# Performance work log

Hardware: AMD Instinct MI355X
Metric: run time of the kernel (lower is better)

Reference implementation:

```python
import jax, jax.numpy as jnp
import numpy as np

LEAKY_SLOPE = 0.01  # torch F.leaky_relu default
LN_EPS = 1e-5       # torch nn.LayerNorm default


def _layer_norm(x, g, b):
    mu = jnp.mean(x, axis=-1, keepdims=True)
    var = jnp.var(x, axis=-1, keepdims=True)
    return (x - mu) * jax.lax.rsqrt(var + LN_EPS) * g + b


def _gcn(x, adj, W, b):
    # GraphConvolution (Kipf-style): adj @ (x @ W) + b
    return adj @ (x @ W) + b


def setup_inputs() -> dict:
    key = jax.random.key(0)
    ks = jax.random.split(key, 8)
    N, fan_in, fan_mid, fan_out = 12288, 128, 128, 20
    h0, h1, h2 = fan_mid, fan_mid // 2, fan_mid // 4  # 128, 64, 32
    inp = {
        "x": jax.random.normal(ks[0], (N, fan_in), dtype=jnp.float32),
        "adj0": jax.random.uniform(ks[1], (N, N), dtype=jnp.float32),
        "adj1": jax.random.uniform(ks[2], (N, N), dtype=jnp.float32),
        "adj2": jax.random.uniform(ks[3], (N, N), dtype=jnp.float32),
        "W0": jax.random.normal(ks[4], (fan_in, h0), dtype=jnp.float32) / np.sqrt(fan_in),
        "b0": jnp.zeros((h0,), dtype=jnp.float32),
        "W1": jax.random.normal(ks[5], (h0, h1), dtype=jnp.float32) / np.sqrt(h0),
        "b1": jnp.zeros((h1,), dtype=jnp.float32),
        "W2": jax.random.normal(ks[6], (h1, h2), dtype=jnp.float32) / np.sqrt(h1),
        "b2": jnp.zeros((h2,), dtype=jnp.float32),
        "g0": jnp.ones((h0,), dtype=jnp.float32),
        "be0": jnp.zeros((h0,), dtype=jnp.float32),
        "g1": jnp.ones((h1,), dtype=jnp.float32),
        "be1": jnp.zeros((h1,), dtype=jnp.float32),
        "g2": jnp.ones((h2,), dtype=jnp.float32),
        "be2": jnp.zeros((h2,), dtype=jnp.float32),
        "Wl": jax.random.normal(ks[7], (h2, fan_out), dtype=jnp.float32) / np.sqrt(h2),
        "bl": jnp.zeros((fan_out,), dtype=jnp.float32),
    }
    return inp


def reference(x, adj0, adj1, adj2, W0, b0, W1, b1, W2, b2,
              g0, be0, g1, be1, g2, be2, Wl, bl):
    # first GCN + LayerNorm (no activation, matching the original forward)
    h = _layer_norm(_gcn(x, adj0, W0, b0), g0, be0)
    # two loop iterations: GCN -> LN -> LeakyReLU -> Dropout(eval=identity)
    h = jax.nn.leaky_relu(_layer_norm(_gcn(h, adj1, W1, b1), g1, be1), LEAKY_SLOPE)
    h = jax.nn.leaky_relu(_layer_norm(_gcn(h, adj2, W2, b2), g2, be2), LEAKY_SLOPE)
    logits = h @ Wl + bl
    return jax.nn.log_softmax(logits, axis=1)
```

## Files before the change

kernel.cpp:

```cpp
#include <hip/hip_runtime.h>
#include <cstdint>
#include <cstddef>

typedef __attribute__((ext_vector_type(8))) short short8;
typedef __attribute__((ext_vector_type(4))) float f32x4;

#define DEV __device__ __forceinline__

DEV unsigned short f2bf(float f) {
  unsigned int u = __float_as_uint(f);
  u += 0x7fffu + ((u >> 16) & 1u);
  return (unsigned short)(u >> 16);
}

DEV unsigned int pk2(float a, float b) {
  return (unsigned int)f2bf(a) | ((unsigned int)f2bf(b) << 16);
}

DEV void glds16(const void* g, void* l) {
  __builtin_amdgcn_global_load_lds(
      (const __attribute__((address_space(1))) void*)g,
      (__attribute__((address_space(3))) void*)l, 16, 0, 0);
}

constexpr int NROW = 12288;

__global__ __launch_bounds__(256) void xw_kernel(
    const float* __restrict__ x, const float* __restrict__ W0,
    unsigned short* __restrict__ t0T) {
  __shared__ float sW[128 * 128];
  __shared__ float sx[16][128];
  const int t = threadIdx.x;
  for (int i = t; i < 128 * 128; i += 256) sW[i] = W0[i];
  const int r0 = blockIdx.x * 16;
  for (int i = t; i < 16 * 128; i += 256)
    sx[i >> 7][i & 127] = x[(size_t)(r0 + (i >> 7)) * 128 + (i & 127)];
  __syncthreads();
  const int c = t & 127;
  const int rg = t >> 7;
  float acc[8] = {0, 0, 0, 0, 0, 0, 0, 0};
  for (int k = 0; k < 128; ++k) {
    float w = sW[k * 128 + c];
#pragma unroll
    for (int j = 0; j < 8; ++j) acc[j] += sx[rg * 8 + j][k] * w;
  }
  uint4 o;
  o.x = pk2(acc[0], acc[1]);
  o.y = pk2(acc[2], acc[3]);
  o.z = pk2(acc[4], acc[5]);
  o.w = pk2(acc[6], acc[7]);
  *(uint4*)(t0T + (size_t)c * NROW + r0 + rg * 8) = o;
}

template <int H>
__global__ __launch_bounds__(256, 3) void gcn_gemm(
    const float* __restrict__ A, const unsigned short* __restrict__ BT,
    float* __restrict__ part) {
  constexpr int KSPLIT = 4;
  constexpr int BM = 64, BK = 64;
  constexpr int WN = (H >= 64) ? 2 : 1;
  constexpr int WM = 4 / WN;
  constexpr int MR = BM / (WM * 16);
  constexpr int NR = H / (WN * 16);
  constexpr int NB = H / 32;
  constexpr int KSTEPS = (NROW / KSPLIT) / BK;
  constexpr int NSUP = KSTEPS / 3;
  constexpr int BBYTES = H * 128;
  static_assert(KSTEPS % 3 == 0, "");

  __shared__ alignas(16) char lds[16384 + 2 * BBYTES];
  char* ldsB = lds + 16384;

  const int t = threadIdx.x;
  const int xcd = blockIdx.x & 7;
  const int idx = blockIdx.x >> 3;
  const int split = xcd >> 1;
  const int bm = ((xcd & 1) ? 96 : 0) + idx;
  const int k0 = split * (NROW / KSPLIT);

  const int r = t >> 2, q = t & 3;
  const float* aptr = A + (size_t)(bm * BM + r) * NROW + k0;
  const int sw = (r & 7) << 4;

  const int nB0 = t >> 3;
  const int wB = (t & 7) ^ (nB0 & 7);
  const unsigned short* bptr = BT + (size_t)nB0 * NROW + k0 + wB * 8;
  const int wid = t >> 6;
  char* ldsBw = ldsB + wid * 1024;

  const int lane = t & 63;
  const int l15 = lane & 15;
  const int loct = lane >> 4;
  const int wm = wid / WN;
  const int wn = wid % WN;
  int aoff[MR][2], boff[NR][2];
#pragma unroll
  for (int m = 0; m < MR; ++m)
#pragma unroll
    for (int kk = 0; kk < 2; ++kk) {
      int row = wm * (MR * 16) + m * 16 + l15;
      aoff[m][kk] = (row * 128 + kk * 64 + loct * 16) ^ ((row & 7) << 4);
    }
#pragma unroll
  for (int n = 0; n < NR; ++n)
#pragma unroll
    for (int kk = 0; kk < 2; ++kk) {
      int nn = wn * (NR * 16) + n * 16 + l15;
      boff[n][kk] = (nn * 128 + kk * 64 + loct * 16) ^ ((nn & 7) << 4);
    }

  f32x4 acc[MR][NR];
#pragma unroll
  for (int m = 0; m < MR; ++m)
#pragma unroll
    for (int n = 0; n < NR; ++n) acc[m][n] = {0.f, 0.f, 0.f, 0.f};

  f32x4 av[12];

  auto issueSuper = [&](int S) {
#pragma unroll
    for (int j = 0; j < 3; ++j)
#pragma unroll
      for (int i = 0; i < 4; ++i)
        av[j * 4 + i] =
            *(const f32x4*)(aptr + S * 192 + j * 64 + i * 16 + q * 4);
  };
  auto glB = [&](int s, int buf) {
#pragma unroll
    for (int j = 0; j < NB; ++j)
      glds16(bptr + (size_t)j * 32 * NROW + s * BK,
             ldsBw + buf * BBYTES + j * 4096);
  };
  auto cvtWrite = [&](int j, int buf) {
    char* wb = lds + buf * 8192;
#pragma unroll
    for (int i = 0; i < 4; ++i) {
      uint2 w;
      w.x = pk2(av[j * 4 + i].x, av[j * 4 + i].y);
      w.y = pk2(av[j * 4 + i].z, av[j * 4 + i].w);
      *(uint2*)(wb + ((r * 128 + i * 32 + q * 8) ^ sw)) = w;
    }
  };
  auto compute = [&](int buf) {
    const char* lA = lds + buf * 8192;
    const char* lB = ldsB + buf * BBYTES;
#pragma unroll
    for (int kk = 0; kk < 2; ++kk) {
      short8 af[MR], bfv[NR];
#pragma unroll
      for (int m = 0; m < MR; ++m) af[m] = *(const short8*)(lA + aoff[m][kk]);
#pragma unroll
      for (int n = 0; n < NR; ++n) bfv[n] = *(const short8*)(lB + boff[n][kk]);
#pragma unroll
      for (int m = 0; m < MR; ++m)
#pragma unroll
        for (int n = 0; n < NR; ++n)
          acc[m][n] = __builtin_amdgcn_mfma_f32_16x16x32_bf16(
              af[m], bfv[n], acc[m][n], 0, 0, 0);
    }
  };

  glB(0, 0);
  __builtin_amdgcn_sched_barrier(0);
  issueSuper(0);
  cvtWrite(0, 0);
  asm volatile("s_waitcnt vmcnt(0) lgkmcnt(0)" ::: "memory");
  __builtin_amdgcn_s_barrier();
  __builtin_amdgcn_sched_barrier(0);

  for (int S = 0; S < NSUP; ++S) {
    const int b = S & 1;
    glB(3 * S + 1, b ^ 1);
    compute(b);
    cvtWrite(1, b ^ 1);
    asm volatile("s_waitcnt vmcnt(0) lgkmcnt(0)" ::: "memory");
    __builtin_amdgcn_s_barrier();
    __builtin_amdgcn_sched_barrier(0);
    glB(3 * S + 2, b);
    __builtin_amdgcn_sched_barrier(0);
    compute(b ^ 1);
    cvtWrite(2, b);
    if (S + 1 < NSUP) {
      issueSuper(S + 1);
      asm volatile("s_waitcnt vmcnt(12) lgkmcnt(0)" ::: "memory");
    } else {
      asm volatile("s_waitcnt vmcnt(0) lgkmcnt(0)" ::: "memory");
    }
    __builtin_amdgcn_s_barrier();
    __builtin_amdgcn_sched_barrier(0);
    if (S + 1 < NSUP) {
      glB(3 * S + 3, b ^ 1);
      compute(b);
      cvtWrite(0, b ^ 1);
      asm volatile("s_waitcnt vmcnt(0) lgkmcnt(0)" ::: "memory");
      __builtin_amdgcn_s_barrier();
      __builtin_amdgcn_sched_barrier(0);
    } else {
      compute(b);
    }
  }

  float* pout = part + ((size_t)split * NROW + (size_t)bm * BM) * H;
#pragma unroll
  for (int m = 0; m < MR; ++m) {
    const int row = wm * (MR * 16) + m * 16 + loct * 4;
#pragma unroll
    for (int n = 0; n < NR; ++n) {
      const int col = wn * (NR * 16) + n * 16 + l15;
#pragma unroll
      for (int rr = 0; rr < 4; ++rr)
        pout[(size_t)(row + rr) * H + col] = acc[m][n][rr];
    }
  }
}

template <int H, int H2, bool ACT>
__global__ __launch_bounds__(256) void reduce_ln(
    const float* __restrict__ part, const float* __restrict__ bias,
    const float* __restrict__ g, const float* __restrict__ be,
    const float* __restrict__ Wn, unsigned short* __restrict__ tT) {
  __shared__ float sW[H * H2];
  __shared__ float sh[4][H];
  const int t = threadIdx.x;
  for (int i = t; i < H * H2; i += 256) sW[i] = Wn[i];
  __syncthreads();

  const int wid = t >> 6, lane = t & 63;
  const int row = blockIdx.x * 4 + wid;
  constexpr int CPL = H / 64;
  float v[CPL];
#pragma unroll
  for (int c = 0; c < CPL; ++c) {
    const int col = lane + c * 64;
    float s = bias[col];
#pragma unroll
    for (int sp = 0; sp < 4; ++sp)
      s += part[((size_t)sp * NROW + row) * H + col];
    v[c] = s;
  }
  float sum = 0;
#pragma unroll
  for (int c = 0; c < CPL; ++c) sum += v[c];
#pragma unroll
  for (int o = 32; o > 0; o >>= 1) sum += __shfl_xor(sum, o);
  const float mu = sum / H;
  float vs = 0;
#pragma unroll
  for (int c = 0; c < CPL; ++c) { float d = v[c] - mu; vs += d * d; }
#pragma unroll
  for (int o = 32; o > 0; o >>= 1) vs += __shfl_xor(vs, o);
  const float rstd = rsqrtf(vs / H + 1e-5f);
#pragma unroll
  for (int c = 0; c < CPL; ++c) {
    const int col = lane + c * 64;
    float h = (v[c] - mu) * rstd * g[col] + be[col];
    if (ACT) h = (h > 0.f) ? h : 0.01f * h;
    sh[wid][col] = h;
  }
  __syncthreads();
  if (lane < H2) {
    float d = 0;
#pragma unroll 8
    for (int k = 0; k < H; ++k) d += sh[wid][k] * sW[k * H2 + lane];
    tT[(size_t)lane * NROW + row] = f2bf(d);
  }
}

__global__ __launch_bounds__(256) void reduce_final(
    const float* __restrict__ part, const float* __restrict__ bias,
    const float* __restrict__ g, const float* __restrict__ be,
    const float* __restrict__ Wl, const float* __restrict__ bl,
    float* __restrict__ out) {
  __shared__ float sW[32 * 20];
  __shared__ float sbl[20];
  __shared__ float sh[4][32];
  __shared__ float sl[4][20];
  const int t = threadIdx.x;
  for (int i = t; i < 640; i += 256) sW[i] = Wl[i];
  if (t < 20) sbl[t] = bl[t];
  __syncthreads();
  const int wid = t >> 6, lane = t & 63;
  const int row = blockIdx.x * 4 + wid;
  const int col = lane & 31;
  float v = bias[col];
#pragma unroll
  for (int sp = 0; sp < 4; ++sp)
    v += part[((size_t)sp * NROW + row) * 32 + col];
  float sum = v;
#pragma unroll
  for (int o = 32; o > 0; o >>= 1) sum += __shfl_xor(sum, o);
  const float mu = sum / 64.f;
  float d0 = v - mu;
  float vs = d0 * d0;
#pragma unroll
  for (int o = 32; o > 0; o >>= 1) vs += __shfl_xor(vs, o);
  const float rstd = rsqrtf(vs / 64.f + 1e-5f);
  float h = (v - mu) * rstd * g[col] + be[col];
  h = (h > 0.f) ? h : 0.01f * h;
  if (lane < 32) sh[wid][col] = h;
  __syncthreads();
  if (lane < 20) {
    float lg = sbl[lane];
#pragma unroll
    for (int k = 0; k < 32; ++k) lg += sh[wid][k] * sW[k * 20 + lane];
    sl[wid][lane] = lg;
  }
  __syncthreads();
  if (lane < 20) {
    float mx = -1e30f;
#pragma unroll
    for (int k = 0; k < 20; ++k) mx = fmaxf(mx, sl[wid][k]);
    float se = 0.f;
#pragma unroll
    for (int k = 0; k < 20; ++k) se += expf(sl[wid][k] - mx);
    out[(size_t)row * 20 + lane] = sl[wid][lane] - mx - logf(se);
  }
}

extern "C" void kernel_launch(void* const* d_in, const int* in_sizes, int n_in,
                              void* d_out, int out_size, void* d_ws,
                              size_t ws_size, hipStream_t stream) {
  const float* x    = (const float*)d_in[0];
  const float* adj0 = (const float*)d_in[1];
  const float* adj1 = (const float*)d_in[2];
  const float* adj2 = (const float*)d_in[3];
  const float* W0   = (const float*)d_in[4];
  const float* b0   = (const float*)d_in[5];
  const float* W1   = (const float*)d_in[6];
  const float* b1   = (const float*)d_in[7];
  const float* W2   = (const float*)d_in[8];
  const float* b2   = (const float*)d_in[9];
  const float* g0   = (const float*)d_in[10];
  const float* be0  = (const float*)d_in[11];
  const float* g1   = (const float*)d_in[12];
  const float* be1  = (const float*)d_in[13];
  const float* g2   = (const float*)d_in[14];
  const float* be2  = (const float*)d_in[15];
  const float* Wl   = (const float*)d_in[16];
  const float* bl   = (const float*)d_in[17];
  float* out = (float*)d_out;

  char* ws = (char*)d_ws;
  float* part =          (float*)(ws);
  unsigned short* t0T = (unsigned short*)(ws + 25165824);
  unsigned short* t1T = (unsigned short*)(ws + 25165824 + 3145728);
  unsigned short* t2T = (unsigned short*)(ws + 25165824 + 3145728 + 1572864);

  xw_kernel<<<NROW / 16, 256, 0, stream>>>(x, W0, t0T);
  gcn_gemm<128><<<(NROW / 64) * 4, 256, 0, stream>>>(adj0, t0T, part);
  reduce_ln<128, 64, false><<<NROW / 4, 256, 0, stream>>>(part, b0, g0, be0, W1, t1T);
  gcn_gemm<64><<<(NROW / 64) * 4, 256, 0, stream>>>(adj1, t1T, part);
  reduce_ln<64, 32, true><<<NROW / 4, 256, 0, stream>>>(part, b1, g1, be1, W2, t2T);
  gcn_gemm<32><<<(NROW / 64) * 4, 256, 0, stream>>>(adj2, t2T, part);
  reduce_final<<<NROW / 4, 256, 0, stream>>>(part, b2, g2, be2, Wl, bl, out);
}
```

Before: 450.1 us.

## Stage B tiles through registers with two-deep prefetch instead of direct global-to-LDS loads

Replaces the global_load_lds path for the bf16 B operand with ordinary vector loads into two register buffers, written to LDS one step later. B loads are issued two K-steps ahead, and barriers now wait only on LDS counters instead of draining all vector memory loads. The aim is to hide global latency for B behind the MFMA compute. In exchange it uses more registers, adds explicit LDS writes, and relies on the compiler inserting correct vmcnt waits before the register-to-LDS writes.

```diff
diff --git a/kernel.cpp b/kernel.cpp
--- a/kernel.cpp
+++ b/kernel.cpp
@@ -15,12 +15,6 @@
 
 DEV unsigned int pk2(float a, float b) {
   return (unsigned int)f2bf(a) | ((unsigned int)f2bf(b) << 16);
-}
-
-DEV void glds16(const void* g, void* l) {
-  __builtin_amdgcn_global_load_lds(
-      (const __attribute__((address_space(1))) void*)g,
-      (__attribute__((address_space(3))) void*)l, 16, 0, 0);
 }
 
 constexpr int NROW = 12288;
@@ -86,7 +80,6 @@
   const int wB = (t & 7) ^ (nB0 & 7);
   const unsigned short* bptr = BT + (size_t)nB0 * NROW + k0 + wB * 8;
   const int wid = t >> 6;
-  char* ldsBw = ldsB + wid * 1024;
 
   const int lane = t & 63;
   const int l15 = lane & 15;
@@ -116,6 +109,7 @@
     for (int n = 0; n < NR; ++n) acc[m][n] = {0.f, 0.f, 0.f, 0.f};
 
   f32x4 av[12];
+  uint4 br0[NB], br1[NB];
 
   auto issueSuper = [&](int S) {
 #pragma unroll
@@ -125,11 +119,16 @@
         av[j * 4 + i] =
             *(const f32x4*)(aptr + S * 192 + j * 64 + i * 16 + q * 4);
   };
-  auto glB = [&](int s, int buf) {
+  auto glBreg = [&](uint4* br, int s) {
+    if (s >= KSTEPS) return;
 #pragma unroll
     for (int j = 0; j < NB; ++j)
-      glds16(bptr + (size_t)j * 32 * NROW + s * BK,
-             ldsBw + buf * BBYTES + j * 4096);
+      br[j] = *(const uint4*)(bptr + (size_t)j * 32 * NROW + s * BK);
+  };
+  auto wrB = [&](const uint4* br, int buf) {
+#pragma unroll
+    for (int j = 0; j < NB; ++j)
+      *(uint4*)(ldsB + buf * BBYTES + j * 4096 + t * 16) = br[j];
   };
   auto cvtWrite = [&](int j, int buf) {
     char* wb = lds + buf * 8192;
@@ -160,45 +159,43 @@
     }
   };
 
-  glB(0, 0);
+#define BARRIER_LG                                         \
+  asm volatile("s_waitcnt lgkmcnt(0)" ::: "memory");       \
+  __builtin_amdgcn_s_barrier();                            \
   __builtin_amdgcn_sched_barrier(0);
+
+  glBreg(br0, 0);
   issueSuper(0);
+  wrB(br0, 0);
+  glBreg(br1, 1);
   cvtWrite(0, 0);
-  asm volatile("s_waitcnt vmcnt(0) lgkmcnt(0)" ::: "memory");
-  __builtin_amdgcn_s_barrier();
-  __builtin_amdgcn_sched_barrier(0);
+  BARRIER_LG;
 
   for (int S = 0; S < NSUP; ++S) {
     const int b = S & 1;
-    glB(3 * S + 1, b ^ 1);
+    const int s = 3 * S;
+    glBreg((s & 1) ? br1 : br0, s + 2);
     compute(b);
+    wrB(((s + 1) & 1) ? br1 : br0, b ^ 1);
     cvtWrite(1, b ^ 1);
-    asm volatile("s_waitcnt vmcnt(0) lgkmcnt(0)" ::: "memory");
-    __builtin_amdgcn_s_barrier();
-    __builtin_amdgcn_sched_barrier(0);
-    glB(3 * S + 2, b);
-    __builtin_amdgcn_sched_barrier(0);
+    BARRIER_LG;
+    glBreg(((s + 1) & 1) ? br1 : br0, s + 3);
     compute(b ^ 1);
+    wrB((s & 1) ? br1 : br0, b);
     cvtWrite(2, b);
+    if (S + 1 < NSUP) issueSuper(S + 1);
+    BARRIER_LG;
     if (S + 1 < NSUP) {
-      issueSuper(S + 1);
-      asm volatile("s_waitcnt vmcnt(12) lgkmcnt(0)" ::: "memory");
-    } else {
-      asm volatile("s_waitcnt vmcnt(0) lgkmcnt(0)" ::: "memory");
-    }
-    __builtin_amdgcn_s_barrier();
-    __builtin_amdgcn_sched_barrier(0);
-    if (S + 1 < NSUP) {
-      glB(3 * S + 3, b ^ 1);
+      glBreg((s & 1) ? br1 : br0, s + 4);
       compute(b);
+      wrB(((s + 1) & 1) ? br1 : br0, b ^ 1);
       cvtWrite(0, b ^ 1);
-      asm volatile("s_waitcnt vmcnt(0) lgkmcnt(0)" ::: "memory");
-      __builtin_amdgcn_s_barrier();
-      __builtin_amdgcn_sched_barrier(0);
+      BARRIER_LG;
     } else {
       compute(b);
     }
   }
+#undef BARRIER_LG
 
   float* pout = part + ((size_t)split * NROW + (size_t)bm * BM) * H;
 #pragma unroll
```

Result: slower. 744.0 us (+65.3%).
